# Kernel tuning notes

Hardware: AMD Instinct MI355X
Metric: run time of the kernel (lower is better)

The kernel has to match this reference:

```python
import jax, jax.numpy as jnp
import numpy as np

B, N, E, H, T, FC = 16, 4096, 131072, 16, 3, 20


def setup_inputs() -> dict:
    key = jax.random.key(0)
    ks = jax.random.split(key, 16)
    F = jnp.eye(3, dtype=jnp.float32)[None] + 0.05 * jax.random.normal(ks[0], (B, 3, 3), dtype=jnp.float32)
    node_pos = jax.random.uniform(ks[1], (N, 3), dtype=jnp.float32)
    edge_src = jax.random.randint(ks[2], (E,), 0, N)
    edge_dst = jax.random.randint(ks[3], (E,), 0, N)
    edge_type = jax.random.randint(ks[4], (E,), 0, T)
    sc = lambda k, s: jax.random.normal(k, s, dtype=jnp.float32) / np.float32(np.sqrt(s[0]))
    return {
        'F': F, 'node_pos': node_pos,
        'edge_src': edge_src, 'edge_dst': edge_dst, 'edge_type': edge_type,
        'W_in': sc(ks[5], (3, H)),
        'fc1_0': sc(ks[6], (T, FC)), 'fc2_0': sc(ks[7], (FC, 1)), 'W_0': sc(ks[8], (H, H)),
        'fc1_1': sc(ks[9], (T, FC)), 'fc2_1': sc(ks[10], (FC, 1)), 'W_1': sc(ks[11], (H, H)),
        'W_out': sc(ks[12], (H, 3)),
        'w': jax.random.uniform(ks[13], (N * N,), dtype=jnp.float32),
    }


def _message_passing(Fx, edge_src, edge_dst, edge_oh,
                     W_in, fc1_0, fc2_0, W_0, fc1_1, fc2_1, W_1, W_out):
    # simplified stand-in for e3nn MessagePassing_v1: per-edge scalar gate from
    # edge-type MLP (fc_neurons=[3,20]), gather-scatter aggregation / sqrt(deg)
    inv_sqrt_deg = np.float32(1.0 / np.sqrt(edge_src.shape[0] / Fx.shape[1]))
    h = Fx @ W_in  # [B,N,H]
    for fc1, fc2, Wl in ((fc1_0, fc2_0, W_0), (fc1_1, fc2_1, W_1)):
        ew = jax.nn.relu(edge_oh @ fc1) @ fc2          # [E,1]
        msg = h[:, edge_src] * ew[None]                # [B,E,H]
        agg = jnp.zeros_like(h).at[:, edge_dst].add(msg) * inv_sqrt_deg
        h = jax.nn.relu(agg @ Wl)
    return h @ W_out  # [B,N,3]


def reference(F, node_pos, edge_src, edge_dst, edge_type,
              W_in, fc1_0, fc2_0, W_0, fc1_1, fc2_1, W_1, W_out, w):
    edge_oh = jax.nn.one_hot(edge_type, T, dtype=F.dtype)
    Fx = jnp.einsum('bij,nj->bni', F, node_pos)                     # deform positions
    h = _message_passing(Fx, edge_src, edge_dst, edge_oh,
                         W_in, fc1_0, fc2_0, W_0, fc1_1, fc2_1, W_1, W_out)
    Fx_ij = h[:, edge_src] - h[:, edge_dst]                         # [B,E,3]
    x_ij = jnp.einsum('bij,bej->bei', jnp.linalg.inv(F), Fx_ij)     # [B,E,3]
    n = node_pos.shape[0]
    a = Fx_ij[:, :n]  # original loop indexes first N edges with node index i
    c = x_ij[:, :n]
    W2 = w.reshape(n, n)
    # vectorized form of: sum_ij w[i*n+j] * kron(Fx_ij[b,i], x_ij[b,j])
    t = jnp.einsum('ij,bip->bjp', W2, a)                            # [B,N,3]
    stress = jnp.einsum('bjp,bjq->bpq', t, c).reshape(F.shape[0], 9)
    return stress
```

## Files before the change

kernel.cpp:

```cpp
#include <hip/hip_runtime.h>

#define N_NODES 4096
#define N_EDGES 131072
#define BATCH   16
#define HDIM    16
#define FCDIM   20
#define BH      256
#define ISD     0.17677669529663687f
#define NSTRIP  32

__device__ __forceinline__ float f4get(const float4& v, int k) {
    return k == 0 ? v.x : (k == 1 ? v.y : (k == 2 ? v.z : v.w));
}

__global__ void setup_kernel(const float* __restrict__ F, const float* __restrict__ W_in,
                             const float* __restrict__ fc1_0, const float* __restrict__ fc2_0,
                             const float* __restrict__ fc1_1, const float* __restrict__ fc2_1,
                             float* __restrict__ ew, float* __restrict__ G,
                             float* __restrict__ invF, float* __restrict__ out144,
                             int* __restrict__ cnt) {
    int t = threadIdx.x;
    if (t < 6) {
        const float* fc1 = (t < 3) ? fc1_0 : fc1_1;
        const float* fc2 = (t < 3) ? fc2_0 : fc2_1;
        int ty = t % 3;
        float s = 0.f;
        for (int f = 0; f < FCDIM; ++f) {
            float v = fc1[ty * FCDIM + f];
            v = v > 0.f ? v : 0.f;
            s += v * fc2[f];
        }
        ew[t] = s;
    }
    for (int idx = t; idx < BATCH * 3 * HDIM; idx += 256) {
        int b = idx / 48, r = idx % 48, j = r / HDIM, k = r % HDIM;
        float s = 0.f;
        for (int i = 0; i < 3; ++i) s += F[b * 9 + i * 3 + j] * W_in[i * HDIM + k];
        G[idx] = s;
    }
    if (t < BATCH) {
        const float* f = F + t * 9;
        float a00=f[0],a01=f[1],a02=f[2],a10=f[3],a11=f[4],a12=f[5],a20=f[6],a21=f[7],a22=f[8];
        float det = a00*(a11*a22-a12*a21) - a01*(a10*a22-a12*a20) + a02*(a10*a21-a11*a20);
        float id = 1.f/det;
        float* o = invF + t*9;
        o[0]=(a11*a22-a12*a21)*id; o[1]=(a02*a21-a01*a22)*id; o[2]=(a01*a12-a02*a11)*id;
        o[3]=(a12*a20-a10*a22)*id; o[4]=(a00*a22-a02*a20)*id; o[5]=(a02*a10-a00*a12)*id;
        o[6]=(a10*a21-a11*a20)*id; o[7]=(a01*a20-a00*a21)*id; o[8]=(a00*a11-a01*a10)*id;
    }
    if (t < 144) out144[t] = 0.f;
    for (int i = t; i < N_NODES; i += 256) cnt[i] = 0;
}

__global__ void h0_hist_kernel(const float* __restrict__ pos, const float* __restrict__ G,
                               float* __restrict__ h0,
                               const int* __restrict__ edst, int* __restrict__ cnt) {
    int bid = blockIdx.x;
    int t = threadIdx.x;
    if (bid < 1024) {
        int id = bid * 256 + t;
        int n  = id >> 6;
        int c4 = (id & 63) << 2;
        int b  = c4 >> 4;
        int k  = c4 & 15;
        float p0 = pos[n*3+0], p1 = pos[n*3+1], p2 = pos[n*3+2];
        const float* g = G + b*48 + k;
        float4 r;
        r.x = p0*g[0] + p1*g[16] + p2*g[32];
        r.y = p0*g[1] + p1*g[17] + p2*g[33];
        r.z = p0*g[2] + p1*g[18] + p2*g[34];
        r.w = p0*g[3] + p1*g[19] + p2*g[35];
        *(float4*)(h0 + n*BH + c4) = r;
    } else {
        int e = (bid - 1024) * 256 + t;
        if (e < N_EDGES) atomicAdd(&cnt[edst[e]], 1);
    }
}

__global__ void scan_kernel(const int* __restrict__ cnt, int* __restrict__ off,
                            int* __restrict__ cursor) {
    __shared__ int wsum[4];
    int t = threadIdx.x;
    int lane = t & 63, wave = t >> 6;
    int base = t * 16;
    int loc[16];
    int s = 0;
    #pragma unroll
    for (int i = 0; i < 16; ++i) { loc[i] = s; s += cnt[base + i]; }
    int pre = s;
    #pragma unroll
    for (int o = 1; o < 64; o <<= 1) {
        int v = __shfl_up(pre, o);
        if (lane >= o) pre += v;
    }
    if (lane == 63) wsum[wave] = pre;
    __syncthreads();
    int woff = 0;
    #pragma unroll
    for (int w = 0; w < 4; ++w) if (w < wave) woff += wsum[w];
    int excl = woff + pre - s;
    #pragma unroll
    for (int i = 0; i < 16; ++i) {
        int v = excl + loc[i];
        off[base + i] = v;
        cursor[base + i] = v;
    }
    if (t == 255) off[N_NODES] = excl + s;
}
__global__ void fill_kernel(const int* __restrict__ src, const int* __restrict__ dst,
                            const int* __restrict__ typ, int* __restrict__ cursor,
                            int* __restrict__ sedge) {
    int e = blockIdx.x * 256 + threadIdx.x;
    if (e < N_EDGES) {
        int p = atomicAdd(&cursor[dst[e]], 1);
        sedge[p] = src[e] | (typ[e] << 16);
    }
}

__global__ void layer_kernel(const float* __restrict__ h_in, float* __restrict__ h_out,
                             const int* __restrict__ off, const int* __restrict__ sedge,
                             const float* __restrict__ ew3, const float* __restrict__ W) {
    __shared__ float Wl[256];
    __shared__ float aggS[2][16*17 + 4];
    int t = threadIdx.x;
    Wl[t] = W[t];
    int wave = t >> 6, lane = t & 63;
    int node = wave >> 1;
    int half = wave & 1;
    int d = blockIdx.x * 2 + node;
    float e0 = ew3[0], e1 = ew3[1], e2 = ew3[2];
    int beg = off[d], end = off[d+1];
    int col = half * 128 + lane * 2;
    float2 acc = {0.f, 0.f};
    int it = beg;
    for (; it + 7 < end; it += 8) {
        int v[8]; float2 hv[8];
        #pragma unroll
        for (int u = 0; u < 8; ++u) v[u] = sedge[it + u];
        #pragma unroll
        for (int u = 0; u < 8; ++u)
            hv[u] = *(const float2*)(h_in + (v[u] & 0xFFFF) * BH + col);
        #pragma unroll
        for (int u = 0; u < 8; ++u) {
            int ty = v[u] >> 16;
            float wg = (ty == 0) ? e0 : (ty == 1 ? e1 : e2);
            acc.x += wg * hv[u].x; acc.y += wg * hv[u].y;
        }
    }
    for (; it < end; ++it) {
        int v = sedge[it];
        int ty = v >> 16;
        float wg = (ty == 0) ? e0 : (ty == 1 ? e1 : e2);
        float2 hv = *(const float2*)(h_in + (v & 0xFFFF) * BH + col);
        acc.x += wg * hv.x; acc.y += wg * hv.y;
    }
    int b = col >> 4, k0 = col & 15;
    aggS[node][b*17 + k0]     = acc.x * ISD;
    aggS[node][b*17 + k0 + 1] = acc.y * ISD;
    __syncthreads();
    int en = t >> 7, c2 = (t & 127) * 2;
    int eb = c2 >> 4, ek = c2 & 15;
    const float* arow = aggS[en] + eb * 17;
    float o0 = 0.f, o1 = 0.f;
    #pragma unroll
    for (int k = 0; k < 16; ++k) {
        float av = arow[k];
        o0 += av * Wl[k*16 + ek];
        o1 += av * Wl[k*16 + ek + 1];
    }
    int ed = blockIdx.x * 2 + en;
    float2 r;
    r.x = o0 > 0.f ? o0 : 0.f;
    r.y = o1 > 0.f ? o1 : 0.f;
    *(float2*)(h_out + ed*BH + c2) = r;
}

__global__ void hout_kernel(const float* __restrict__ h2, const float* __restrict__ Wout,
                            float* __restrict__ hout) {
    __shared__ float Wo[48];
    int t = threadIdx.x;
    if (t < 48) Wo[t] = Wout[t];
    __syncthreads();
    int id = blockIdx.x * 256 + t;
    int n = id >> 4, b = id & 15;
    const float* hr = h2 + n*BH + b*HDIM;
    float s0=0.f, s1=0.f, s2=0.f;
    #pragma unroll
    for (int k = 0; k < 16; ++k) {
        float v = hr[k];
        s0 += v*Wo[k*3+0]; s1 += v*Wo[k*3+1]; s2 += v*Wo[k*3+2];
    }
    float* o = hout + n*48 + b*3;
    o[0]=s0; o[1]=s1; o[2]=s2;
}

__global__ void ac_kernel(const float* __restrict__ hout, const int* __restrict__ esrc,
                          const int* __restrict__ edst, const float* __restrict__ invF,
                          float* __restrict__ a, float* __restrict__ c) {
    __shared__ float iF[144];
    int t = threadIdx.x;
    if (t < 144) iF[t] = invF[t];
    __syncthreads();
    int id = blockIdx.x * 256 + t;
    int i = id >> 4, b = id & 15;
    int s = esrc[i], d = edst[i];
    float a0 = hout[s*48+b*3+0] - hout[d*48+b*3+0];
    float a1 = hout[s*48+b*3+1] - hout[d*48+b*3+1];
    float a2 = hout[s*48+b*3+2] - hout[d*48+b*3+2];
    float* ap = a + i*48 + b*3;
    ap[0]=a0; ap[1]=a1; ap[2]=a2;
    const float* m = iF + b*9;
    float* cp = c + i*48 + b*3;
    cp[0] = m[0]*a0 + m[1]*a1 + m[2]*a2;
    cp[1] = m[3]*a0 + m[4]*a1 + m[5]*a2;
    cp[2] = m[6]*a0 + m[7]*a1 + m[8]*a2;
}

__global__ __launch_bounds__(1024, 4)
void tmat_kernel(const float* __restrict__ W2, const float* __restrict__ a,
                 float* __restrict__ partial) {
    __shared__ float sacc[48 * 256];
    int t = threadIdx.x;
    int lane = t & 63;
    int wave = t >> 6;
    int cw   = wave & 3;
    int rg   = wave >> 2;
    int cg   = cw * 12;
    int jb    = (blockIdx.x & 15) * 256;
    int strip = blockIdx.x >> 4;
    int i0    = strip * 128 + rg * 32;
    int jloc  = lane * 4;
    int j     = jb + jloc;
    const float* w2p = W2 + (size_t)i0 * N_NODES + j;
    const float* ap  = a + (size_t)i0 * 48 + cg;
    float4 acc[4][3];
    #pragma unroll
    for (int jj = 0; jj < 4; ++jj)
        #pragma unroll
        for (int q = 0; q < 3; ++q) acc[jj][q] = make_float4(0.f,0.f,0.f,0.f);
    for (int ii = 0; ii < 32; ii += 8) {
        float4 w[8];
        #pragma unroll
        for (int u = 0; u < 8; ++u)
            w[u] = *(const float4*)(w2p + (size_t)(ii + u) * N_NODES);
        #pragma unroll
        for (int u = 0; u < 8; ++u) {
            const float* ar = ap + (size_t)(ii + u) * 48;
            float4 x = *(const float4*)(ar);
            float4 y = *(const float4*)(ar + 4);
            float4 z = *(const float4*)(ar + 8);
            #pragma unroll
            for (int jj = 0; jj < 4; ++jj) {
                float wv = f4get(w[u], jj);
                acc[jj][0].x += wv*x.x; acc[jj][0].y += wv*x.y;
                acc[jj][0].z += wv*x.z; acc[jj][0].w += wv*x.w;
                acc[jj][1].x += wv*y.x; acc[jj][1].y += wv*y.y;
                acc[jj][1].z += wv*y.z; acc[jj][1].w += wv*y.w;
                acc[jj][2].x += wv*z.x; acc[jj][2].y += wv*z.y;
                acc[jj][2].z += wv*z.z; acc[jj][2].w += wv*z.w;
            }
        }
    }
    #pragma unroll 1
    for (int g = 0; g < 4; ++g) {
        if (rg == g) {
            #pragma unroll
            for (int c = 0; c < 12; ++c) {
                float4* p = (float4*)&sacc[(cg + c) * 256 + jloc];
                float4 v;
                v.x = f4get(acc[0][c >> 2], c & 3);
                v.y = f4get(acc[1][c >> 2], c & 3);
                v.z = f4get(acc[2][c >> 2], c & 3);
                v.w = f4get(acc[3][c >> 2], c & 3);
                if (g == 0) *p = v;
                else { float4 o = *p; o.x+=v.x; o.y+=v.y; o.z+=v.z; o.w+=v.w; *p = o; }
            }
        }
        __syncthreads();
    }
    float* pbase = partial + (size_t)strip * (48 * N_NODES);
    #pragma unroll
    for (int k = 0; k < 3; ++k) {
        int f = k * 1024 + t;
        int col = f >> 6;
        int jl  = (f & 63) * 4;
        float4 v = *(float4*)&sacc[col * 256 + jl];
        *(float4*)(pbase + (size_t)col * N_NODES + jb + jl) = v;
    }
}

__global__ void reduce_kernel(const float* __restrict__ partial, float* __restrict__ tmat) {
    int x = (blockIdx.x * 64 + threadIdx.x) * 4;
    float4 s = {0.f, 0.f, 0.f, 0.f};
    #pragma unroll 4
    for (int st = 0; st < NSTRIP; ++st) {
        float4 v = *(const float4*)(partial + (size_t)st * (48 * N_NODES) + x);
        s.x += v.x; s.y += v.y; s.z += v.z; s.w += v.w;
    }
    *(float4*)(tmat + x) = s;
}

__global__ void stress2_kernel(const float* __restrict__ tmat, const float* __restrict__ c,
                               float* __restrict__ out) {
    __shared__ float shred[256 * 9];
    int t = threadIdx.x;
    int b = t & 15, jl = t >> 4;
    int jbase = blockIdx.x * 64;
    float s[9];
    #pragma unroll
    for (int r = 0; r < 9; ++r) s[r] = 0.f;
    for (int pass = 0; pass < 4; ++pass) {
        int j = jbase + pass * 16 + jl;
        float t0 = tmat[(size_t)(b*3+0) * N_NODES + j];
        float t1 = tmat[(size_t)(b*3+1) * N_NODES + j];
        float t2 = tmat[(size_t)(b*3+2) * N_NODES + j];
        const float* cp = c + (size_t)j * 48 + b * 3;
        float c0 = cp[0], c1 = cp[1], c2 = cp[2];
        s[0] += t0*c0; s[1] += t0*c1; s[2] += t0*c2;
        s[3] += t1*c0; s[4] += t1*c1; s[5] += t1*c2;
        s[6] += t2*c0; s[7] += t2*c1; s[8] += t2*c2;
    }
    #pragma unroll
    for (int r = 0; r < 9; ++r) shred[t * 9 + r] = s[r];
    __syncthreads();
    if (t < 144) {
        int bb = t / 9, r = t % 9;
        float acc = 0.f;
        #pragma unroll
        for (int g = 0; g < 16; ++g)
            acc += shred[(g * 16 + bb) * 9 + r];
        atomicAdd(&out[t], acc);
    }
}

extern "C" void kernel_launch(void* const* d_in, const int* in_sizes, int n_in,
                              void* d_out, int out_size, void* d_ws, size_t ws_size,
                              hipStream_t stream) {
    const float* F     = (const float*)d_in[0];
    const float* pos   = (const float*)d_in[1];
    const int*   esrc  = (const int*)d_in[2];
    const int*   edst  = (const int*)d_in[3];
    const int*   etyp  = (const int*)d_in[4];
    const float* W_in  = (const float*)d_in[5];
    const float* fc1_0 = (const float*)d_in[6];
    const float* fc2_0 = (const float*)d_in[7];
    const float* W_0   = (const float*)d_in[8];
    const float* fc1_1 = (const float*)d_in[9];
    const float* fc2_1 = (const float*)d_in[10];
    const float* W_1   = (const float*)d_in[11];
    const float* W_out = (const float*)d_in[12];
    const float* w2    = (const float*)d_in[13];
    float* out = (float*)d_out;

    float* ws   = (float*)d_ws;
    float* ew   = ws;
    float* G    = ws + 16;
    float* invF = ws + 800;
    float* bufA = ws + 1024;
    float* bufB = bufA + N_NODES*BH;
    float* hout = bufB + N_NODES*BH;
    float* aArr = hout + N_NODES*48;
    float* cArr = aArr + N_NODES*48;
    float* tmat = cArr + N_NODES*48;
    int* cnt    = (int*)(tmat + N_NODES*48);
    int* off    = cnt + N_NODES;
    int* cursor = off + N_NODES + 1;
    int* sedge  = cursor + N_NODES;
    float* partial = (float*)(sedge + N_EDGES);

    setup_kernel<<<1, 256, 0, stream>>>(F, W_in, fc1_0, fc2_0, fc1_1, fc2_1, ew, G, invF, out, cnt);
    h0_hist_kernel<<<1536, 256, 0, stream>>>(pos, G, bufA, edst, cnt);
    scan_kernel<<<1, 256, 0, stream>>>(cnt, off, cursor);
    fill_kernel<<<512, 256, 0, stream>>>(esrc, edst, etyp, cursor, sedge);
    layer_kernel<<<2048, 256, 0, stream>>>(bufA, bufB, off, sedge, ew,     W_0);
    layer_kernel<<<2048, 256, 0, stream>>>(bufB, bufA, off, sedge, ew + 3, W_1);
    hout_kernel<<<256, 256, 0, stream>>>(bufA, W_out, hout);
    ac_kernel<<<256, 256, 0, stream>>>(hout, esrc, edst, invF, aArr, cArr);
    tmat_kernel<<<512, 1024, 0, stream>>>(w2, aArr, partial);
    reduce_kernel<<<768, 64, 0, stream>>>(partial, tmat);
    stress2_kernel<<<64, 256, 0, stream>>>(tmat, cArr, out);
}
```

Measured before the change: 232.0 us.

## Restructure tmat kernel: 256-thread blocks, LDS-staged a, double-buffered W2 loads

```diff
diff --git a/kernel.cpp b/kernel.cpp
--- a/kernel.cpp
+++ b/kernel.cpp
@@ -216,42 +216,51 @@
     cp[2] = m[6]*a0 + m[7]*a1 + m[8]*a2;
 }
 
-__global__ __launch_bounds__(1024, 4)
+__global__ __launch_bounds__(256, 2)
 void tmat_kernel(const float* __restrict__ W2, const float* __restrict__ a,
                  float* __restrict__ partial) {
-    __shared__ float sacc[48 * 256];
+    __shared__ float sa[128 * 48];
     int t = threadIdx.x;
     int lane = t & 63;
     int wave = t >> 6;
-    int cw   = wave & 3;
-    int rg   = wave >> 2;
-    int cg   = cw * 12;
+    int cg   = wave * 12;
     int jb    = (blockIdx.x & 15) * 256;
     int strip = blockIdx.x >> 4;
-    int i0    = strip * 128 + rg * 32;
-    int jloc  = lane * 4;
-    int j     = jb + jloc;
+    int i0    = strip * 128;
+    {
+        const float4* ga = (const float4*)(a + (size_t)i0 * 48);
+        float4* la = (float4*)sa;
+        #pragma unroll
+        for (int k = 0; k < 6; ++k) la[t + k * 256] = ga[t + k * 256];
+    }
+    __syncthreads();
+    int j = jb + lane * 4;
     const float* w2p = W2 + (size_t)i0 * N_NODES + j;
-    const float* ap  = a + (size_t)i0 * 48 + cg;
     float4 acc[4][3];
     #pragma unroll
     for (int jj = 0; jj < 4; ++jj)
         #pragma unroll
         for (int q = 0; q < 3; ++q) acc[jj][q] = make_float4(0.f,0.f,0.f,0.f);
-    for (int ii = 0; ii < 32; ii += 8) {
-        float4 w[8];
-        #pragma unroll
-        for (int u = 0; u < 8; ++u)
-            w[u] = *(const float4*)(w2p + (size_t)(ii + u) * N_NODES);
-        #pragma unroll
-        for (int u = 0; u < 8; ++u) {
-            const float* ar = ap + (size_t)(ii + u) * 48;
+    float4 wA[8], wB[8];
+    #pragma unroll
+    for (int u = 0; u < 8; ++u)
+        wA[u] = *(const float4*)(w2p + (size_t)u * N_NODES);
+    #pragma unroll 1
+    for (int base = 0; base < 128; base += 16) {
+        #pragma unroll
+        for (int u = 0; u < 8; ++u) {
+            int r = base + 8 + u;
+            wB[u] = *(const float4*)(w2p + (size_t)r * N_NODES);
+        }
+        #pragma unroll
+        for (int u = 0; u < 8; ++u) {
+            const float* ar = &sa[(base + u) * 48 + cg];
             float4 x = *(const float4*)(ar);
             float4 y = *(const float4*)(ar + 4);
             float4 z = *(const float4*)(ar + 8);
             #pragma unroll
             for (int jj = 0; jj < 4; ++jj) {
-                float wv = f4get(w[u], jj);
+                float wv = f4get(wA[u], jj);
                 acc[jj][0].x += wv*x.x; acc[jj][0].y += wv*x.y;
                 acc[jj][0].z += wv*x.z; acc[jj][0].w += wv*x.w;
                 acc[jj][1].x += wv*y.x; acc[jj][1].y += wv*y.y;
@@ -260,32 +269,38 @@
                 acc[jj][2].z += wv*z.z; acc[jj][2].w += wv*z.w;
             }
         }
-    }
-    #pragma unroll 1
-    for (int g = 0; g < 4; ++g) {
-        if (rg == g) {
+        #pragma unroll
+        for (int u = 0; u < 8; ++u) {
+            int r = base + 16 + u; if (r > 127) r = 127;
+            wA[u] = *(const float4*)(w2p + (size_t)r * N_NODES);
+        }
+        #pragma unroll
+        for (int u = 0; u < 8; ++u) {
+            const float* ar = &sa[(base + 8 + u) * 48 + cg];
+            float4 x = *(const float4*)(ar);
+            float4 y = *(const float4*)(ar + 4);
+            float4 z = *(const float4*)(ar + 8);
             #pragma unroll
-            for (int c = 0; c < 12; ++c) {
-                float4* p = (float4*)&sacc[(cg + c) * 256 + jloc];
-                float4 v;
-                v.x = f4get(acc[0][c >> 2], c & 3);
-                v.y = f4get(acc[1][c >> 2], c & 3);
-                v.z = f4get(acc[2][c >> 2], c & 3);
-                v.w = f4get(acc[3][c >> 2], c & 3);
-                if (g == 0) *p = v;
-                else { float4 o = *p; o.x+=v.x; o.y+=v.y; o.z+=v.z; o.w+=v.w; *p = o; }
+            for (int jj = 0; jj < 4; ++jj) {
+                float wv = f4get(wB[u], jj);
+                acc[jj][0].x += wv*x.x; acc[jj][0].y += wv*x.y;
+                acc[jj][0].z += wv*x.z; acc[jj][0].w += wv*x.w;
+                acc[jj][1].x += wv*y.x; acc[jj][1].y += wv*y.y;
+                acc[jj][1].z += wv*y.z; acc[jj][1].w += wv*y.w;
+                acc[jj][2].x += wv*z.x; acc[jj][2].y += wv*z.y;
+                acc[jj][2].z += wv*z.z; acc[jj][2].w += wv*z.w;
             }
         }
-        __syncthreads();
-    }
-    float* pbase = partial + (size_t)strip * (48 * N_NODES);
-    #pragma unroll
-    for (int k = 0; k < 3; ++k) {
-        int f = k * 1024 + t;
-        int col = f >> 6;
-        int jl  = (f & 63) * 4;
-        float4 v = *(float4*)&sacc[col * 256 + jl];
-        *(float4*)(pbase + (size_t)col * N_NODES + jb + jl) = v;
+    }
+    float* pbase = partial + (size_t)strip * (48 * N_NODES) + jb;
+    #pragma unroll
+    for (int c = 0; c < 12; ++c) {
+        float4 v;
+        v.x = f4get(acc[0][c >> 2], c & 3);
+        v.y = f4get(acc[1][c >> 2], c & 3);
+        v.z = f4get(acc[2][c >> 2], c & 3);
+        v.w = f4get(acc[3][c >> 2], c & 3);
+        *(float4*)(pbase + (size_t)(cg + c) * N_NODES + lane * 4) = v;
     }
 }
 
@@ -376,7 +391,7 @@
     layer_kernel<<<2048, 256, 0, stream>>>(bufB, bufA, off, sedge, ew + 3, W_1);
     hout_kernel<<<256, 256, 0, stream>>>(bufA, W_out, hout);
     ac_kernel<<<256, 256, 0, stream>>>(hout, esrc, edst, invF, aArr, cArr);
-    tmat_kernel<<<512, 1024, 0, stream>>>(w2, aArr, partial);
+    tmat_kernel<<<512, 256, 0, stream>>>(w2, aArr, partial);
     reduce_kernel<<<768, 64, 0, stream>>>(partial, tmat);
     stress2_kernel<<<64, 256, 0, stream>>>(tmat, cArr, out);
 }
```

Measured after the change: 230.6 us. About the same (-0.6%).
